# Optimization experiments

Hardware: AMD Instinct MI355X
Metric: run time of the kernel (lower is better)

The kernel has to match this reference:

```python
import jax, jax.numpy as jnp
import numpy as np

# PyG RGATConv defaults: attention_mechanism='across-relation',
# attention_mode='additive-self-attention', dim=1, negative_slope=0.2.
# Dropout is a no-op in eval mode (reference is deterministic).
HEADS = 8
OUT = 64          # hidden_size (per-head out_channels)
R = 8             # num_relations
NEG_SLOPE = 0.2


def segment_softmax(logits, seg, num_segments):
    # PyG softmax: stable per-destination-node softmax with +1e-16 in denom
    m = jax.ops.segment_max(logits, seg, num_segments=num_segments)
    ex = jnp.exp(logits - m[seg])
    s = jax.ops.segment_sum(ex, seg, num_segments=num_segments)
    return ex / (s[seg] + 1e-16)


def rgat_layer(x, src, dst, etype, eattr, W, q, k, We, e, bias, concat, num_nodes):
    # W: [R, F_in, HEADS*OUT]. Transform all nodes under every relation once,
    # then gather per edge -- same math as x_j @ W[edge_type] but avoids the
    # huge [E, F_in, H*OUT] per-edge weight gather.
    t = jnp.einsum('nf,rfh->rnh', x, W)           # [R, N, H*OUT]
    qn = t @ q                                    # [R, N, HEADS] (dim=1)
    kn = t @ k                                    # [R, N, HEADS]
    qi = qn[etype, dst]                           # [E, HEADS]
    kj = kn[etype, src]                           # [E, HEADS]
    ae = (eattr @ We) @ e                         # [E, HEADS] edge-attr fusion
    alpha = jax.nn.leaky_relu(qi + kj + ae, NEG_SLOPE)
    alpha = segment_softmax(alpha, dst, num_nodes)           # across-relation softmax
    out_j = t[etype, src].reshape(-1, HEADS, OUT)            # [E, H, OUT]
    agg = jax.ops.segment_sum(alpha[:, :, None] * out_j, dst,
                              num_segments=num_nodes)        # [N, H, OUT]
    out = agg.reshape(num_nodes, HEADS * OUT) if concat else agg.mean(axis=1)
    return out + bias


def setup_inputs() -> dict:
    key = jax.random.key(0)
    ks = jax.random.split(key, 16)
    N, E, F = 16000, 256000, 256
    H = HEADS * OUT  # 512

    def p(k, shape, fan_in):
        return jax.random.normal(k, shape, jnp.float32) * np.float32(1.0 / np.sqrt(fan_in))

    return dict(
        x=jax.random.normal(ks[0], (N, F), jnp.float32),
        edge_index=jax.random.randint(ks[1], (2, E), 0, N, dtype=jnp.int32),
        edge_type=jax.random.randint(ks[2], (E,), 0, R, dtype=jnp.int32),
        edge_attr=jax.random.uniform(ks[3], (E, 1), jnp.float32),
        W1=p(ks[4], (R, F, H), F), q1=p(ks[5], (H, HEADS), H), k1=p(ks[6], (H, HEADS), H),
        We1=p(ks[7], (1, H), 1), e1=p(ks[8], (H, HEADS), H), b1=jnp.zeros((H,), jnp.float32),
        W2=p(ks[9], (R, H, H), H), q2=p(ks[10], (H, HEADS), H), k2=p(ks[11], (H, HEADS), H),
        We2=p(ks[12], (1, H), 1), e2=p(ks[13], (H, HEADS), H), b2=jnp.zeros((OUT,), jnp.float32),
    )


def reference(x, edge_index, edge_type, edge_attr,
              W1, q1, k1, We1, e1, b1,
              W2, q2, k2, We2, e2, b2):
    N = x.shape[0]
    # add_self_loops with edge_attr fill_value=0.5
    loop = jnp.arange(N, dtype=edge_index.dtype)
    src = jnp.concatenate([edge_index[0], loop])
    dst = jnp.concatenate([edge_index[1], loop])
    ea = jnp.concatenate([edge_attr, jnp.full((N, edge_attr.shape[1]), 0.5, edge_attr.dtype)])
    # self-loop edge type = (max(edge_type)+1) % num_relations
    slt = jnp.mod(edge_type.max() + 1, R).astype(edge_type.dtype)
    et = jnp.concatenate([edge_type, jnp.full((N,), 1, edge_type.dtype) * slt])

    h = rgat_layer(x, src, dst, et, ea, W1, q1, k1, We1, e1, b1, True, N)    # [N, H*OUT]
    out = rgat_layer(h, src, dst, et, ea, W2, q2, k2, We2, e2, b2, False, N)  # [N, OUT]
    return out
```

## Files before the change

### kernel.cpp

```cpp
#include <hip/hip_runtime.h>
#include <hip/hip_bf16.h>
#include <cstdint>
#include <cstddef>

#define NN 16000
#define MPAD 16128
#define EE 256000
#define ETOT (EE + NN)
#define RREL 8
#define NHEAD 8
#define DOUT 64
#define HD 512
#define NEG 0.2f
#define NMAIN 1008
#define NBH 1063
#define NBA 4000
#define NBW1 129
#define NBB1 256
#define NBATT 4000
#define NBB2 512
#define NBW2 257

typedef unsigned int u32;
typedef short bf16x8 __attribute__((ext_vector_type(8)));
typedef float f32x4 __attribute__((ext_vector_type(4)));

__device__ inline unsigned short f2bf(float f) {
  u32 i = __float_as_uint(f);
  u32 r = (i + 0x7fff + ((i >> 16) & 1)) >> 16;
  return (unsigned short)r;
}
__device__ inline float bf2f(unsigned short h) {
  return __uint_as_float((u32)h << 16);
}
__device__ inline void g2lds16(const void* g, void* lds) {
  __builtin_amdgcn_global_load_lds(
      (const __attribute__((address_space(1))) unsigned int*)g,
      (__attribute__((address_space(3))) unsigned int*)lds, 16, 0, 0);
}

__device__ __forceinline__ void dev_hist(int bid, const int* __restrict__ ei,
                                         const int* __restrict__ et,
                                         int* __restrict__ deg, int* meta) {
  int e = bid * 256 + (int)threadIdx.x;
  if (e >= ETOT) return;
  int dst;
  if (e < EE) { dst = ei[EE + e]; atomicMax(&meta[0], et[e]); }
  else dst = e - EE;
  atomicAdd(&deg[dst], 1);
}

__device__ __forceinline__ void dev_asplit(int bid, const float* __restrict__ in,
                                           unsigned short* __restrict__ A2, int F) {
  long idx = (long)bid * 256 + threadIdx.x;
  long total = (long)NN * (F >> 2);
  if (idx >= total) return;
  int row = (int)(idx / (F >> 2));
  int c4 = (int)(idx % (F >> 2)) << 2;
  float4 v = *(const float4*)&in[(size_t)row * F + c4];
  ushort4 hi;
  hi.x = f2bf(v.x); hi.y = f2bf(v.y); hi.z = f2bf(v.z); hi.w = f2bf(v.w);
  *(ushort4*)&A2[(size_t)row * F + c4] = hi;
}

__device__ __forceinline__ void dev_wqk(int bid, int nmain, const float* __restrict__ W,
                                        const float* __restrict__ q,
                                        const float* __restrict__ k,
                                        const float* __restrict__ We,
                                        const float* __restrict__ e,
                                        unsigned short* __restrict__ WQKT,
                                        float* __restrict__ cvec, int F) {
  if (bid == nmain) {
    int j = threadIdx.x;
    if (j < NHEAD) {
      float acc = 0.f;
      for (int h2 = 0; h2 < HD; ++h2) acc += We[h2] * e[h2 * NHEAD + j];
      cvec[j] = acc;
    }
    return;
  }
  int g = bid * 256 + (int)threadIdx.x;
  int j = g & 15;
  int rf = g >> 4;
  int f = rf % F;
  const float* wrow = W + (size_t)rf * HD;
  const float* qk = ((j < 8) ? q : k) + (j & 7);
  float acc = 0.f;
  for (int h = 0; h < HD; ++h) acc += wrow[h] * qk[(size_t)h * NHEAD];
  const int col = (rf / F) * 16 + j;
  WQKT[(size_t)col * F + f] = f2bf(acc);
}

__device__ void dev_bsplit(int f0b, int c0b, int r, const float* __restrict__ W,
                           unsigned short* __restrict__ BT, int F,
                           float (*tile)[65]) {
  const int f0 = f0b * 64, c0 = c0b * 64;
  int tid = threadIdx.x;
  int i0 = tid >> 6;
  int j = tid & 63;
  const float* Wr = W + (size_t)r * F * 512;
  for (int i = i0; i < 64; i += 4)
    tile[i][j] = Wr[(size_t)(f0 + i) * 512 + c0 + j];
  __syncthreads();
  unsigned short* Br = BT + (size_t)r * 512 * F;
  for (int c = i0; c < 64; c += 4) {
    float v = tile[j][c];
    Br[(size_t)(c0 + c) * F + f0 + j] = f2bf(v);
  }
}

__device__ __forceinline__ void dev_attn1(int bid, const unsigned short* __restrict__ t,
    const float* __restrict__ qkbuf, const float* __restrict__ cvec,
    const int* __restrict__ rowptr, const int* __restrict__ csr_src,
    const int* __restrict__ csr_et, const float* __restrict__ csr_ea,
    const float* __restrict__ bias, unsigned short* __restrict__ A2out) {
  const int wv = threadIdx.x >> 6;
  const int lane = threadIdx.x & 63;
  const int n = bid * 4 + wv;
  const int h = lane >> 3;
  const int c0 = lane << 3;
  const int e0 = rowptr[n], e1 = rowptr[n + 1];
  const float ch = cvec[h];
  const float* qrow = qkbuf + (size_t)n * 128;
  float m = -1e30f, l = 0.f;
  float acc[8] = {};
  int rN = csr_et[e0];
  float aN = csr_ea[e0];
  int sN = csr_src[e0];
  uint4 tvN = *(const uint4*)&t[((size_t)rN * MPAD + sN) * HD + c0];
  float klogN = qkbuf[(size_t)sN * 128 + rN * 16 + 8 + h];
  for (int e = e0; e < e1; ++e) {
    const int r = rN;
    const float a = aN;
    const uint4 tv = tvN;
    const float klog = klogN;
    const float qv = qrow[r * 16 + h];
    if (e + 1 < e1) {
      const int s2 = csr_src[e + 1];
      rN = csr_et[e + 1];
      aN = csr_ea[e + 1];
      tvN = *(const uint4*)&t[((size_t)rN * MPAD + s2) * HD + c0];
      klogN = qkbuf[(size_t)s2 * 128 + rN * 16 + 8 + h];
    }
    float logit = qv + klog + a * ch;
    logit = (logit > 0.f) ? logit : NEG * logit;
    float p;
    if (logit <= m) {
      p = __expf(logit - m);
    } else {
      const float sc = __expf(m - logit);
      l *= sc;
#pragma unroll
      for (int c = 0; c < 8; ++c) acc[c] *= sc;
      m = logit;
      p = 1.f;
    }
    l += p;
    acc[0] = fmaf(p, __uint_as_float((tv.x & 0xffffu) << 16), acc[0]);
    acc[1] = fmaf(p, __uint_as_float(tv.x & 0xffff0000u), acc[1]);
    acc[2] = fmaf(p, __uint_as_float((tv.y & 0xffffu) << 16), acc[2]);
    acc[3] = fmaf(p, __uint_as_float(tv.y & 0xffff0000u), acc[3]);
    acc[4] = fmaf(p, __uint_as_float((tv.z & 0xffffu) << 16), acc[4]);
    acc[5] = fmaf(p, __uint_as_float(tv.z & 0xffff0000u), acc[5]);
    acc[6] = fmaf(p, __uint_as_float((tv.w & 0xffffu) << 16), acc[6]);
    acc[7] = fmaf(p, __uint_as_float(tv.w & 0xffff0000u), acc[7]);
  }
  const float inv = 1.f / (l + 1e-16f);
  unsigned short his[8];
#pragma unroll
  for (int c = 0; c < 8; ++c)
    his[c] = f2bf(fmaf(acc[c], inv, bias[c0 + c]));
  uint4 wh;
  wh.x = (u32)his[0] | ((u32)his[1] << 16);
  wh.y = (u32)his[2] | ((u32)his[3] << 16);
  wh.z = (u32)his[4] | ((u32)his[5] << 16);
  wh.w = (u32)his[6] | ((u32)his[7] << 16);
  *(uint4*)&A2out[(size_t)n * 512 + c0] = wh;
}

__global__ __launch_bounds__(256) void k_prep1(const int* __restrict__ ei,
    const int* __restrict__ et, int* __restrict__ deg, int* meta,
    const float* __restrict__ x, unsigned short* __restrict__ A2,
    const float* __restrict__ W1, const float* __restrict__ q1,
    const float* __restrict__ k1, const float* __restrict__ We1,
    const float* __restrict__ e1, unsigned short* __restrict__ WQKT,
    float* __restrict__ cvec1, unsigned short* __restrict__ BT) {
  __shared__ float tile[64][65];
  int b = blockIdx.x;
  if (b < NBH) { dev_hist(b, ei, et, deg, meta); return; }
  b -= NBH;
  if (b < NBA) { dev_asplit(b, x, A2, 256); return; }
  b -= NBA;
  if (b < NBW1) { dev_wqk(b, NBW1 - 1, W1, q1, k1, We1, e1, WQKT, cvec1, 256); return; }
  b -= NBW1;
  dev_bsplit(b & 3, (b >> 2) & 7, b >> 5, W1, BT, 256, tile);
}

__global__ __launch_bounds__(256) void k_attn1f(const unsigned short* __restrict__ t,
    const float* __restrict__ qkbuf, const float* __restrict__ cvec1,
    const int* __restrict__ rowptr, const int* __restrict__ csr_src,
    const int* __restrict__ csr_et, const float* __restrict__ csr_ea,
    const float* __restrict__ b1, unsigned short* __restrict__ A2out,
    const float* __restrict__ W2, const float* __restrict__ q2,
    const float* __restrict__ k2, const float* __restrict__ We2,
    const float* __restrict__ e2, unsigned short* __restrict__ WQKT,
    float* __restrict__ cvec2, unsigned short* __restrict__ BT) {
  __shared__ float tile[64][65];
  int b = blockIdx.x;
  if (b < NBATT) {
    dev_attn1(b, t, qkbuf, cvec1, rowptr, csr_src, csr_et, csr_ea, b1, A2out);
    return;
  }
  b -= NBATT;
  if (b < NBB2) { dev_bsplit(b & 7, (b >> 3) & 7, b >> 6, W2, BT, 512, tile); return; }
  b -= NBB2;
  dev_wqk(b, NBW2 - 1, W2, q2, k2, We2, e2, WQKT, cvec2, 512);
}

__global__ __launch_bounds__(1024) void k_scan(const int* __restrict__ deg,
                                               int* __restrict__ rowptr,
                                               int* __restrict__ fill) {
  __shared__ int sm[1024];
  const int tid = threadIdx.x;
  const int base = tid * 16;
  int local[16];
  int s = 0;
#pragma unroll
  for (int i = 0; i < 16; ++i) {
    int idx = base + i;
    int v = (idx < NN) ? deg[idx] : 0;
    local[i] = s;
    s += v;
  }
  sm[tid] = s;
  __syncthreads();
  for (int off = 1; off < 1024; off <<= 1) {
    int t = (tid >= off) ? sm[tid - off] : 0;
    __syncthreads();
    sm[tid] += t;
    __syncthreads();
  }
  const int pre = (tid > 0) ? sm[tid - 1] : 0;
#pragma unroll
  for (int i = 0; i < 16; ++i) {
    int idx = base + i;
    if (idx < NN) { rowptr[idx] = pre + local[i]; fill[idx] = pre + local[i]; }
  }
  if (tid == 1023) rowptr[NN] = sm[1023];
}

__global__ void k_scatter(const int* __restrict__ ei, const int* __restrict__ et,
                          const float* __restrict__ ea, const int* __restrict__ meta,
                          int* __restrict__ fill, int* __restrict__ csr_src,
                          int* __restrict__ csr_et, float* __restrict__ csr_ea) {
  int e = blockIdx.x * 256 + threadIdx.x;
  if (e >= ETOT) return;
  int src, dst, r; float a;
  if (e < EE) { src = ei[e]; dst = ei[EE + e]; r = et[e]; a = ea[e]; }
  else { src = dst = e - EE; r = (meta[0] + 1) & (RREL - 1); a = 0.5f; }
  int pos = atomicAdd(&fill[dst], 1);
  csr_src[pos] = src; csr_et[pos] = r; csr_ea[pos] = a;
}

__global__ __launch_bounds__(512, 2) void k_mgemm(const unsigned short* __restrict__ A2,
                                                  const unsigned short* __restrict__ BT,
                                                  const unsigned short* __restrict__ WQKT,
                                                  unsigned short* __restrict__ Ct,
                                                  float* __restrict__ qkbuf,
                                                  int Kp) {
  const int bid = blockIdx.x;
  const bool isqk = (bid >= NMAIN);
  int m0, n0;
  const unsigned short* Bbase;
  if (!isqk) {
    const int v = (bid & 7) * 126 + (bid >> 3);
    m0 = (v >> 4) << 8;
    n0 = (v & 15) << 8;
    Bbase = BT;
  } else {
    m0 = (bid - NMAIN) << 8;
    n0 = 0;
    Bbase = WQKT;
  }

  __shared__ __align__(16) unsigned short smem[49152];

  const int tid = threadIdx.x;
  const int wid = tid >> 6;
  const int lane = tid & 63;
  const int wr = wid >> 2;
  const int wc = wid & 3;
  const int rlow = lane & 15;
  const int kch = lane >> 4;

  const unsigned short* srcA[2];
  const unsigned short* srcB[2];
  int dstOff[2];
#pragma unroll
  for (int p = 0; p < 2; ++p) {
    int fr = (p << 3) + wid;
    srcA[p] = A2 + (size_t)(m0 + fr * 16 + rlow) * Kp + kch * 8;
    srcB[p] = Bbase + (size_t)(n0 + fr * 16 + rlow) * Kp + kch * 8;
    dstOff[p] = fr * 512;
  }

  f32x4 acc[8][4] = {};
  const int nt = Kp >> 5;

#pragma unroll
  for (int tp = 0; tp < 2; ++tp) {
    const int ko = tp << 5;
#pragma unroll
    for (int p = 0; p < 2; ++p) {
      g2lds16(srcA[p] + ko, &smem[tp * 8192 + dstOff[p]]);
      g2lds16(srcB[p] + ko, &smem[24576 + tp * 8192 + dstOff[p]]);
    }
  }

  int buf = 0;
  for (int u = 0; u < nt; ++u) {
    if (u + 1 < nt)
      asm volatile("s_waitcnt vmcnt(4)" ::: "memory");
    else
      asm volatile("s_waitcnt vmcnt(0)" ::: "memory");
    __builtin_amdgcn_s_barrier();
    asm volatile("" ::: "memory");
    if (u + 2 < nt) {
      int nb2 = buf + 2; if (nb2 >= 3) nb2 -= 3;
      const int ko = (u + 2) << 5;
#pragma unroll
      for (int p = 0; p < 2; ++p) {
        g2lds16(srcA[p] + ko, &smem[nb2 * 8192 + dstOff[p]]);
        g2lds16(srcB[p] + ko, &smem[24576 + nb2 * 8192 + dstOff[p]]);
      }
    }
    const unsigned short* Ab = smem + buf * 8192;
    const unsigned short* Bb = smem + 24576 + buf * 8192;
    bf16x8 af[8], bv[4];
#pragma unroll
    for (int i = 0; i < 8; ++i)
      af[i] = *(const bf16x8*)&Ab[(wr * 8 + i) * 512 + lane * 8];
#pragma unroll
    for (int j = 0; j < 4; ++j)
      bv[j] = *(const bf16x8*)&Bb[(wc * 4 + j) * 512 + lane * 8];
    __builtin_amdgcn_s_setprio(1);
#pragma unroll
    for (int i = 0; i < 8; ++i)
#pragma unroll
      for (int j = 0; j < 4; ++j)
        acc[i][j] = __builtin_amdgcn_mfma_f32_16x16x32_bf16(af[i], bv[j],
                                                            acc[i][j], 0, 0, 0);
    __builtin_amdgcn_s_setprio(0);
    buf = (buf == 2) ? 0 : buf + 1;
  }

  if (!isqk) {
    __syncthreads();
    float* epsW = (float*)smem + wid * 1344;
    const int rowL = lane & 15;
    const int cseg = lane >> 4;
    const int colfull0 = n0 + wc * 64;
    const int rr = colfull0 >> 9;
    const int hbase = (colfull0 & 511) + cseg * 16;
#pragma unroll
    for (int i = 0; i < 8; ++i) {
#pragma unroll
      for (int j = 0; j < 4; ++j)
        *(f32x4*)&epsW[(j * 16 + rlow) * 21 + kch * 4] = acc[i][j];
      float vals[16];
#pragma unroll
      for (int c = 0; c < 16; ++c) vals[c] = epsW[(cseg * 16 + c) * 21 + rowL];
      const int rowg = m0 + wr * 128 + i * 16 + rowL;
      unsigned short* dst = Ct + ((size_t)rr * MPAD + rowg) * HD + hbase;
      uint4 w0, w1;
      w0.x = (u32)f2bf(vals[0])  | ((u32)f2bf(vals[1])  << 16);
      w0.y = (u32)f2bf(vals[2])  | ((u32)f2bf(vals[3])  << 16);
      w0.z = (u32)f2bf(vals[4])  | ((u32)f2bf(vals[5])  << 16);
      w0.w = (u32)f2bf(vals[6])  | ((u32)f2bf(vals[7])  << 16);
      w1.x = (u32)f2bf(vals[8])  | ((u32)f2bf(vals[9])  << 16);
      w1.y = (u32)f2bf(vals[10]) | ((u32)f2bf(vals[11]) << 16);
      w1.z = (u32)f2bf(vals[12]) | ((u32)f2bf(vals[13]) << 16);
      w1.w = (u32)f2bf(vals[14]) | ((u32)f2bf(vals[15]) << 16);
      *(uint4*)dst = w0;
      *(uint4*)(dst + 8) = w1;
    }
  } else {
    if (wc < 2) {
#pragma unroll
      for (int i = 0; i < 8; ++i) {
        const int row0 = m0 + wr * 128 + i * 16 + kch * 4;
#pragma unroll
        for (int j = 0; j < 4; ++j) {
          const int col = wc * 64 + j * 16 + rlow;
#pragma unroll
          for (int q = 0; q < 4; ++q) {
            const int row = row0 + q;
            if (row < NN) qkbuf[(size_t)row * 128 + col] = acc[i][j][q];
          }
        }
      }
    }
  }
}

__global__ __launch_bounds__(256) void k_attn0(const unsigned short* __restrict__ t,
    const float* __restrict__ qkbuf, const float* __restrict__ cvec,
    const int* __restrict__ rowptr, const int* __restrict__ csr_src,
    const int* __restrict__ csr_et, const float* __restrict__ csr_ea,
    const float* __restrict__ bias, float* __restrict__ out) {
  const int wv = threadIdx.x >> 6;
  const int lane = threadIdx.x & 63;
  const int n = blockIdx.x * 4 + wv;
  const int h = lane >> 3;
  const int c0 = lane << 3;
  const int e0 = rowptr[n], e1 = rowptr[n + 1];
  const float ch = cvec[h];
  const float* qrow = qkbuf + (size_t)n * 128;
  float m = -1e30f, l = 0.f;
  float acc[8] = {};
  int rN = csr_et[e0];
  float aN = csr_ea[e0];
  int sN = csr_src[e0];
  uint4 tvN = *(const uint4*)&t[((size_t)rN * MPAD + sN) * HD + c0];
  float klogN = qkbuf[(size_t)sN * 128 + rN * 16 + 8 + h];
  for (int e = e0; e < e1; ++e) {
    const int r = rN;
    const float a = aN;
    const uint4 tv = tvN;
    const float klog = klogN;
    const float qv = qrow[r * 16 + h];
    if (e + 1 < e1) {
      const int s2 = csr_src[e + 1];
      rN = csr_et[e + 1];
      aN = csr_ea[e + 1];
      tvN = *(const uint4*)&t[((size_t)rN * MPAD + s2) * HD + c0];
      klogN = qkbuf[(size_t)s2 * 128 + rN * 16 + 8 + h];
    }
    float logit = qv + klog + a * ch;
    logit = (logit > 0.f) ? logit : NEG * logit;
    float p;
    if (logit <= m) {
      p = __expf(logit - m);
    } else {
      const float sc = __expf(m - logit);
      l *= sc;
#pragma unroll
      for (int c = 0; c < 8; ++c) acc[c] *= sc;
      m = logit;
      p = 1.f;
    }
    l += p;
    acc[0] = fmaf(p, __uint_as_float((tv.x & 0xffffu) << 16), acc[0]);
    acc[1] = fmaf(p, __uint_as_float(tv.x & 0xffff0000u), acc[1]);
    acc[2] = fmaf(p, __uint_as_float((tv.y & 0xffffu) << 16), acc[2]);
    acc[3] = fmaf(p, __uint_as_float(tv.y & 0xffff0000u), acc[3]);
    acc[4] = fmaf(p, __uint_as_float((tv.z & 0xffffu) << 16), acc[4]);
    acc[5] = fmaf(p, __uint_as_float(tv.z & 0xffff0000u), acc[5]);
    acc[6] = fmaf(p, __uint_as_float((tv.w & 0xffffu) << 16), acc[6]);
    acc[7] = fmaf(p, __uint_as_float(tv.w & 0xffff0000u), acc[7]);
  }
  const float inv = 1.f / (l + 1e-16f);
  __shared__ float sm[4][HD];
#pragma unroll
  for (int c = 0; c < 8; ++c) sm[wv][c0 + c] = acc[c] * inv;
  __syncthreads();
  const int d = lane;
  float s = 0.f;
#pragma unroll
  for (int hh = 0; hh < NHEAD; ++hh) s += sm[wv][hh * 64 + d];
  out[(size_t)n * DOUT + d] = s * 0.125f + bias[d];
}

extern "C" void kernel_launch(void* const* d_in, const int* in_sizes, int n_in,
                              void* d_out, int out_size, void* d_ws, size_t ws_size,
                              hipStream_t stream) {
  const float* x   = (const float*)d_in[0];
  const int*   ei  = (const int*)d_in[1];
  const int*   et  = (const int*)d_in[2];
  const float* ea  = (const float*)d_in[3];
  const float* W1  = (const float*)d_in[4];
  const float* q1  = (const float*)d_in[5];
  const float* k1  = (const float*)d_in[6];
  const float* We1 = (const float*)d_in[7];
  const float* e1  = (const float*)d_in[8];
  const float* b1  = (const float*)d_in[9];
  const float* W2  = (const float*)d_in[10];
  const float* q2  = (const float*)d_in[11];
  const float* k2  = (const float*)d_in[12];
  const float* We2 = (const float*)d_in[13];
  const float* e2  = (const float*)d_in[14];
  const float* b2  = (const float*)d_in[15];
  float* out = (float*)d_out;

  char* w = (char*)d_ws;
  auto alloc = [&](size_t bytes) {
    char* p = w;
    w += (bytes + 255) & ~(size_t)255;
    return p;
  };
  float* qkbuf  = (float*)alloc((size_t)NN * 128 * 4);
  unsigned short* WQKT = (unsigned short*)alloc((size_t)256 * HD * 2);
  unsigned short* A2 = (unsigned short*)alloc((size_t)MPAD * HD * 2);
  unsigned short* BT = (unsigned short*)alloc((size_t)RREL * HD * HD * 2);
  float* cvec1  = (float*)alloc(64);
  float* cvec2  = (float*)alloc(64);
  int*   meta   = (int*)alloc(64);
  int*   deg    = (int*)alloc((size_t)NN * 4);
  int*   rowptr = (int*)alloc((size_t)(NN + 1) * 4);
  int*   fill   = (int*)alloc((size_t)NN * 4);
  int*   csr_src= (int*)alloc((size_t)ETOT * 4);
  int*   csr_et = (int*)alloc((size_t)ETOT * 4);
  float* csr_ea = (float*)alloc((size_t)ETOT * 4);
  unsigned short* t = (unsigned short*)alloc((size_t)RREL * MPAD * HD * 2);
  (void)ws_size;

  (void)hipMemsetAsync(meta, 0, 4, stream);
  (void)hipMemsetAsync(deg, 0, (size_t)NN * 4, stream);
  k_prep1<<<NBH + NBA + NBW1 + NBB1, 256, 0, stream>>>(
      ei, et, deg, meta, x, A2, W1, q1, k1, We1, e1, WQKT, cvec1, BT);
  k_scan<<<1, 1024, 0, stream>>>(deg, rowptr, fill);
  k_scatter<<<(ETOT + 255) / 256, 256, 0, stream>>>(ei, et, ea, meta, fill,
                                                    csr_src, csr_et, csr_ea);
  k_mgemm<<<NMAIN + 63, 512, 0, stream>>>(A2, BT, WQKT, t, qkbuf, 256);
  k_attn1f<<<NBATT + NBB2 + NBW2, 256, 0, stream>>>(
      t, qkbuf, cvec1, rowptr, csr_src, csr_et, csr_ea, b1, A2,
      W2, q2, k2, We2, e2, WQKT, cvec2, BT);
  k_mgemm<<<NMAIN + 63, 512, 0, stream>>>(A2, BT, WQKT, t, qkbuf, 512);
  k_attn0<<<NN / 4, 256, 0, stream>>>(t, qkbuf, cvec2, rowptr, csr_src, csr_et,
                                      csr_ea, b2, out);
}
```

Baseline: 467.9 us.

## Fuse CSR scatter into first GEMM launch and cut GEMM to double buffering

The edge scatter kernel is folded into the first k_mgemm launch as extra tail blocks, which removes one kernel launch and lets the scatter overlap with GEMM tiles. The GEMM pipeline goes from triple to double buffering, shrinking shared memory from 96KB to 64KB, and launch bounds are raised to request 4 blocks per SM. The aim is higher occupancy and less launch overhead, at the cost of a shallower prefetch (a full vmcnt(0) wait each step) and likely register pressure under the tighter launch bound. The scatter blocks sit in a kernel sized for 512 threads with large LDS, so they may occupy slots awkwardly.

```diff
diff --git a/kernel.cpp b/kernel.cpp
--- a/kernel.cpp
+++ b/kernel.cpp
@@ -13,6 +13,8 @@
 #define HD 512
 #define NEG 0.2f
 #define NMAIN 1008
+#define NQK 63
+#define NSCAT 532
 #define NBH 1063
 #define NBA 4000
 #define NBW1 129
@@ -249,26 +251,31 @@
   if (tid == 1023) rowptr[NN] = sm[1023];
 }
 
-__global__ void k_scatter(const int* __restrict__ ei, const int* __restrict__ et,
-                          const float* __restrict__ ea, const int* __restrict__ meta,
-                          int* __restrict__ fill, int* __restrict__ csr_src,
-                          int* __restrict__ csr_et, float* __restrict__ csr_ea) {
-  int e = blockIdx.x * 256 + threadIdx.x;
-  if (e >= ETOT) return;
-  int src, dst, r; float a;
-  if (e < EE) { src = ei[e]; dst = ei[EE + e]; r = et[e]; a = ea[e]; }
-  else { src = dst = e - EE; r = (meta[0] + 1) & (RREL - 1); a = 0.5f; }
-  int pos = atomicAdd(&fill[dst], 1);
-  csr_src[pos] = src; csr_et[pos] = r; csr_ea[pos] = a;
-}
-
-__global__ __launch_bounds__(512, 2) void k_mgemm(const unsigned short* __restrict__ A2,
+__global__ __launch_bounds__(512, 4) void k_mgemm(const unsigned short* __restrict__ A2,
                                                   const unsigned short* __restrict__ BT,
                                                   const unsigned short* __restrict__ WQKT,
                                                   unsigned short* __restrict__ Ct,
                                                   float* __restrict__ qkbuf,
-                                                  int Kp) {
+                                                  int Kp,
+                                                  const int* __restrict__ ei,
+                                                  const int* __restrict__ et,
+                                                  const float* __restrict__ ea,
+                                                  const int* __restrict__ meta,
+                                                  int* __restrict__ fill,
+                                                  int* __restrict__ csr_src,
+                                                  int* __restrict__ csr_et,
+                                                  float* __restrict__ csr_ea) {
   const int bid = blockIdx.x;
+  if (bid >= NMAIN + NQK) {
+    int e = (bid - NMAIN - NQK) * 512 + (int)threadIdx.x;
+    if (e >= ETOT) return;
+    int src, dst, r; float a;
+    if (e < EE) { src = ei[e]; dst = ei[EE + e]; r = et[e]; a = ea[e]; }
+    else { src = dst = e - EE; r = (meta[0] + 1) & (RREL - 1); a = 0.5f; }
+    int pos = atomicAdd(&fill[dst], 1);
+    csr_src[pos] = src; csr_et[pos] = r; csr_ea[pos] = a;
+    return;
+  }
   const bool isqk = (bid >= NMAIN);
   int m0, n0;
   const unsigned short* Bbase;
@@ -283,7 +290,7 @@
     Bbase = WQKT;
   }
 
-  __shared__ __align__(16) unsigned short smem[49152];
+  __shared__ __align__(16) unsigned short smem[32768];
 
   const int tid = threadIdx.x;
   const int wid = tid >> 6;
@@ -308,34 +315,27 @@
   const int nt = Kp >> 5;
 
 #pragma unroll
-  for (int tp = 0; tp < 2; ++tp) {
-    const int ko = tp << 5;
-#pragma unroll
-    for (int p = 0; p < 2; ++p) {
-      g2lds16(srcA[p] + ko, &smem[tp * 8192 + dstOff[p]]);
-      g2lds16(srcB[p] + ko, &smem[24576 + tp * 8192 + dstOff[p]]);
-    }
-  }
-
-  int buf = 0;
+  for (int p = 0; p < 2; ++p) {
+    g2lds16(srcA[p], &smem[dstOff[p]]);
+    g2lds16(srcB[p], &smem[16384 + dstOff[p]]);
+  }
+
   for (int u = 0; u < nt; ++u) {
-    if (u + 1 < nt)
-      asm volatile("s_waitcnt vmcnt(4)" ::: "memory");
-    else
-      asm volatile("s_waitcnt vmcnt(0)" ::: "memory");
+    asm volatile("s_waitcnt vmcnt(0)" ::: "memory");
     __builtin_amdgcn_s_barrier();
     asm volatile("" ::: "memory");
-    if (u + 2 < nt) {
-      int nb2 = buf + 2; if (nb2 >= 3) nb2 -= 3;
-      const int ko = (u + 2) << 5;
+    const int buf = u & 1;
+    if (u + 1 < nt) {
+      const int ko = (u + 1) << 5;
+      const int bo = (buf ^ 1) * 8192;
 #pragma unroll
       for (int p = 0; p < 2; ++p) {
-        g2lds16(srcA[p] + ko, &smem[nb2 * 8192 + dstOff[p]]);
-        g2lds16(srcB[p] + ko, &smem[24576 + nb2 * 8192 + dstOff[p]]);
+        g2lds16(srcA[p] + ko, &smem[bo + dstOff[p]]);
+        g2lds16(srcB[p] + ko, &smem[16384 + bo + dstOff[p]]);
       }
     }
     const unsigned short* Ab = smem + buf * 8192;
-    const unsigned short* Bb = smem + 24576 + buf * 8192;
+    const unsigned short* Bb = smem + 16384 + buf * 8192;
     bf16x8 af[8], bv[4];
 #pragma unroll
     for (int i = 0; i < 8; ++i)
@@ -351,7 +351,6 @@
         acc[i][j] = __builtin_amdgcn_mfma_f32_16x16x32_bf16(af[i], bv[j],
                                                             acc[i][j], 0, 0, 0);
     __builtin_amdgcn_s_setprio(0);
-    buf = (buf == 2) ? 0 : buf + 1;
   }
 
   if (!isqk) {
@@ -519,13 +518,15 @@
   k_prep1<<<NBH + NBA + NBW1 + NBB1, 256, 0, stream>>>(
       ei, et, deg, meta, x, A2, W1, q1, k1, We1, e1, WQKT, cvec1, BT);
   k_scan<<<1, 1024, 0, stream>>>(deg, rowptr, fill);
-  k_scatter<<<(ETOT + 255) / 256, 256, 0, stream>>>(ei, et, ea, meta, fill,
-                                                    csr_src, csr_et, csr_ea);
-  k_mgemm<<<NMAIN + 63, 512, 0, stream>>>(A2, BT, WQKT, t, qkbuf, 256);
+  k_mgemm<<<NMAIN + NQK + NSCAT, 512, 0, stream>>>(
+      A2, BT, WQKT, t, qkbuf, 256, ei, et, ea, meta, fill,
+      csr_src, csr_et, csr_ea);
   k_attn1f<<<NBATT + NBB2 + NBW2, 256, 0, stream>>>(
       t, qkbuf, cvec1, rowptr, csr_src, csr_et, csr_ea, b1, A2,
       W2, q2, k2, We2, e2, WQKT, cvec2, BT);
-  k_mgemm<<<NMAIN + 63, 512, 0, stream>>>(A2, BT, WQKT, t, qkbuf, 512);
+  k_mgemm<<<NMAIN + NQK, 512, 0, stream>>>(
+      A2, BT, WQKT, t, qkbuf, 512, ei, et, ea, meta, fill,
+      csr_src, csr_et, csr_ea);
   k_attn0<<<NN / 4, 256, 0, stream>>>(t, qkbuf, cvec2, rowptr, csr_src, csr_et,
                                       csr_ea, b2, out);
 }
```

New measurement: 1.560 ms. +233.5%, slower.
